# Optimization experiments

Measured on AMD Instinct MI355X. Metric: run time of the kernel, lower is better.

The kernel has to match this reference:

```python
import jax, jax.numpy as jnp
import numpy as np

B, A, F, D, C = 256, 128, 512, 6, 512  # batch, max_atoms, atom_features, max_degree, conv_width


def setup_inputs() -> dict:
    key = jax.random.key(0)
    k1, k2, k3, k4 = jax.random.split(key, 4)
    atoms = jax.random.normal(k1, (B, A, F), dtype=jnp.float32)
    # neighbour indices in [0, A); pad entries beyond each atom's degree with -1
    neigh = jax.random.randint(k2, (B, A, D), 0, A)
    deg = jax.random.randint(k3, (B, A, 1), 0, D)  # degrees in 0..D-1
    bonds = jnp.where(jnp.arange(D)[None, None, :] < deg, neigh, -1)
    # one Dense(conv_width) per degree: stacked kernels [D, F, C] and biases [D, C]
    W = jax.random.normal(k4, (D, F, C), dtype=jnp.float32) * 0.02
    b = jnp.zeros((D, C), dtype=jnp.float32)
    return {"atoms": atoms, "bonds": bonds, "W": W, "b": b}


def reference(atoms, bonds, W, b):
    d_max = bonds.shape[-1]
    # per-atom degree = count of non -1 neighbour slots  [B, A, 1]
    degrees = jnp.sum(bonds != -1, axis=-1, keepdims=True)
    # shift lookup by 1 so that padded (-1) neighbours index a zero row
    padded = jnp.pad(atoms, ((0, 0), (1, 1), (0, 0)))  # [B, A+2, F]
    idx = bonds + 1  # [B, A, D]
    # per-sample gather of neighbour features -> [B, A, D, F]
    neigh_feats = jax.vmap(lambda ref, i: ref[i])(padded, idx)
    summed = jnp.sum(neigh_feats, axis=2) + atoms  # [B, A, F]
    # apply all degree-specific dense layers, then mask-select by degree
    dense = jnp.einsum('baf,dfc->badc', summed, W) + b  # [B, A, D, C]
    masks = (degrees[..., None] == jnp.arange(d_max).reshape(1, 1, d_max, 1)).astype(dense.dtype)
    return jnp.sum(dense * masks, axis=2)  # [B, A, C]
```

## Files before the change

### kernel.cpp

```cpp
#include <hip/hip_runtime.h>
#include <hip/hip_bf16.h>


#define NB 256
#define NA 128
#define NF 512
#define ND 6
#define NC 512
#define NATOMS (NB * NA)

typedef __attribute__((ext_vector_type(8))) short frag8;
typedef __attribute__((ext_vector_type(4))) float f32x4;

static __device__ inline unsigned short f2bu(float f) {
    __hip_bfloat16 h = __float2bfloat16(f);
    return *reinterpret_cast<unsigned short*>(&h);
}
static __device__ inline unsigned int pack2(float a, float b) {
    return (unsigned int)f2bu(a) | ((unsigned int)f2bu(b) << 16);
}
static __device__ inline void async16(const void* g, void* l) {
    __builtin_amdgcn_global_load_lds(
        (const __attribute__((address_space(1))) void*)g,
        (__attribute__((address_space(3))) void*)l, 16, 0, 0);
}

#define PREP_T 1536
#define PREP_B (PREP_T + 32)
#define PREP_S (PREP_B + NATOMS / 4)

__global__ __launch_bounds__(256) void prep(
    const float* __restrict__ atoms, const int* __restrict__ bonds,
    const float* __restrict__ W, __hip_bfloat16* __restrict__ Wt,
    __hip_bfloat16* __restrict__ summed, int* __restrict__ counts,
    int* __restrict__ bucket) {
    const int blk = blockIdx.x;
    const int tid = threadIdx.x;

    if (blk < PREP_T) {
        __shared__ float t[32][33];
        const int tx = tid & 31, ty = tid >> 5;
        const int d   = blk >> 8;
        const int rem = blk & 255;
        const int c0  = (rem & 15) * 32;
        const int f0  = (rem >> 4) * 32;
        #pragma unroll
        for (int r = 0; r < 32; r += 8)
            t[ty + r][tx] = W[((size_t)(d * NF + f0 + ty + r)) * NC + c0 + tx];
        __syncthreads();
        #pragma unroll
        for (int r = 0; r < 32; r += 8)
            Wt[((size_t)(d * NC + c0 + ty + r)) * NF + f0 + tx] =
                __float2bfloat16(t[tx][ty + r]);
    } else if (blk < PREP_B) {
        __shared__ int lcnt[ND];
        __shared__ int lbase[ND];
        const int b = blk - PREP_T;
        if (tid < ND) lcnt[tid] = 0;
        __syncthreads();
        int deg[4], loc[4], gg[4];
        #pragma unroll
        for (int i = 0; i < 4; ++i) {
            int g = b * 1024 + i * 256 + tid;
            gg[i] = g;
            int dg = 0;
            #pragma unroll
            for (int j = 0; j < ND; ++j) dg += (bonds[g * ND + j] >= 0);
            deg[i] = dg;
            loc[i] = atomicAdd(&lcnt[dg], 1);
        }
        __syncthreads();
        if (tid < ND) lbase[tid] = atomicAdd(&counts[tid], lcnt[tid]);
        __syncthreads();
        #pragma unroll
        for (int i = 0; i < 4; ++i)
            bucket[deg[i] * NATOMS + lbase[deg[i]] + loc[i]] = gg[i];
    } else {
        const int wave = tid >> 6;
        const int lane = tid & 63;
        const int g    = (blk - PREP_B) * 4 + wave;
        const float4* a4 = (const float4*)atoms;

        int   nb[ND];
        float msk[ND];
        #pragma unroll
        for (int j = 0; j < ND; ++j) {
            int n = bonds[g * ND + j];
            msk[j] = (n >= 0) ? 1.0f : 0.0f;
            nb[j]  = (n >= 0) ? n : 0;
        }
        const int rowbase = g & ~(NA - 1);

        float4 s0 = a4[(size_t)g * 128 + 2 * lane];
        float4 s1 = a4[(size_t)g * 128 + 2 * lane + 1];
        float4 v0[ND], v1[ND];
        #pragma unroll
        for (int j = 0; j < ND; ++j) {
            const size_t base = (size_t)(rowbase + nb[j]) * 128 + 2 * lane;
            v0[j] = a4[base];
            v1[j] = a4[base + 1];
        }
        #pragma unroll
        for (int j = 0; j < ND; ++j) {
            s0.x = fmaf(v0[j].x, msk[j], s0.x); s0.y = fmaf(v0[j].y, msk[j], s0.y);
            s0.z = fmaf(v0[j].z, msk[j], s0.z); s0.w = fmaf(v0[j].w, msk[j], s0.w);
            s1.x = fmaf(v1[j].x, msk[j], s1.x); s1.y = fmaf(v1[j].y, msk[j], s1.y);
            s1.z = fmaf(v1[j].z, msk[j], s1.z); s1.w = fmaf(v1[j].w, msk[j], s1.w);
        }
        uint4 o;
        o.x = pack2(s0.x, s0.y); o.y = pack2(s0.z, s0.w);
        o.z = pack2(s1.x, s1.y); o.w = pack2(s1.z, s1.w);
        ((uint4*)summed)[(size_t)g * 64 + lane] = o;
    }
}

__global__ __launch_bounds__(256, 4) void gemm_deg(
    const __hip_bfloat16* __restrict__ summed, const __hip_bfloat16* __restrict__ Wt,
    const float* __restrict__ bias, const int* __restrict__ counts,
    const int* __restrict__ bucket, float* __restrict__ out) {
    const int bx = blockIdx.x;
    const int d  = bx % ND;
    const int n0 = (bx / ND) * 128;
    const int Md = counts[d];
    const int m0 = blockIdx.y * 128;
    if (m0 >= Md) return;

    __shared__ __align__(16) __hip_bfloat16 sA[2][128 * 32];
    __shared__ __align__(16) __hip_bfloat16 sB[2][128 * 32];
    __shared__ int sRows[128];

    const int tid = threadIdx.x;
    if (tid < 128) {
        int r = m0 + tid;
        sRows[tid] = (r < Md) ? bucket[d * NATOMS + r] : -1;
    }
    __syncthreads();

    const int lane = tid & 63;
    const int w    = tid >> 6;

    const int slot = lane & 3;
    int   rowc[2];
    size_t gA[2];
    int   segoff[2];
    #pragma unroll
    for (int c = 0; c < 2; ++c) {
        rowc[c] = c * 64 + w * 16 + (lane >> 2);
        int q = sRows[rowc[c]];
        gA[c] = (size_t)((q < 0) ? 0 : q) * (NF * 2);
        segoff[c] = (slot ^ ((rowc[c] >> 1) & 3)) * 16;
    }
    const char* smB = (const char*)summed;
    const char* wtB = (const char*)Wt + (size_t)(d * NC + n0) * (NF * 2);

    const int quad = lane >> 4, l16 = lane & 15;
    const int wy = w >> 1, wx = w & 1;

    f32x4 acc[4][4];
    #pragma unroll
    for (int i = 0; i < 4; ++i)
        #pragma unroll
        for (int j = 0; j < 4; ++j) acc[i][j] = (f32x4)0.0f;

    int offA[4], offB[4];
    #pragma unroll
    for (int i = 0; i < 4; ++i) {
        const int Ra = wy * 64 + i * 16 + l16;
        offA[i] = Ra * 32 + (quad ^ ((Ra >> 1) & 3)) * 8;
        const int Rb = wx * 64 + i * 16 + l16;
        offB[i] = Rb * 32 + (quad ^ ((Rb >> 1) & 3)) * 8;
    }

    #define STAGE(kt, p)                                                         \
        {                                                                        \
            const int kb = (kt) * 64;     \
            _Pragma("unroll")                                                    \
            for (int c = 0; c < 2; ++c) {                                        \
                async16(smB + gA[c] + kb + segoff[c],                            \
                        &sA[p][c * 2048 + w * 512]);                             \
                async16(wtB + (size_t)rowc[c] * (NF * 2) + kb + segoff[c],       \
                        &sB[p][c * 2048 + w * 512]);                             \
            }                                                                    \
        }

    STAGE(0, 0)
    #pragma unroll
    for (int kt = 0; kt < 16; ++kt) {
        const int p = kt & 1;
        __syncthreads();
        if (kt < 15) STAGE(kt + 1, 1 - p)
        frag8 aF[4], bF[4];
        #pragma unroll
        for (int i = 0; i < 4; ++i) aF[i] = *(const frag8*)&sA[p][offA[i]];
        #pragma unroll
        for (int j = 0; j < 4; ++j) bF[j] = *(const frag8*)&sB[p][offB[j]];
        #pragma unroll
        for (int i = 0; i < 4; ++i)
            #pragma unroll
            for (int j = 0; j < 4; ++j)
                acc[i][j] = __builtin_amdgcn_mfma_f32_16x16x32_bf16(
                    aF[i], bF[j], acc[i][j], 0, 0, 0);
    }
    #undef STAGE

    #pragma unroll
    for (int j = 0; j < 4; ++j) {
        const int n = n0 + wx * 64 + j * 16 + l16;
        const float bv = bias[d * NC + n];
        #pragma unroll
        for (int i = 0; i < 4; ++i) {
            #pragma unroll
            for (int r = 0; r < 4; ++r) {
                const int tr = wy * 64 + i * 16 + quad * 4 + r;
                const int g  = sRows[tr];
                if (g >= 0)
                    out[(size_t)g * NC + n] = acc[i][j][r] + bv;
            }
        }
    }
}

extern "C" void kernel_launch(void* const* d_in, const int* in_sizes, int n_in,
                              void* d_out, int out_size, void* d_ws, size_t ws_size,
                              hipStream_t stream) {
    const float* atoms = (const float*)d_in[0];
    const int*   bonds = (const int*)d_in[1];
    const float* W     = (const float*)d_in[2];
    const float* bias  = (const float*)d_in[3];
    float* out = (float*)d_out;

    char* ws = (char*)d_ws;
    int* counts = (int*)ws;
    int* bucket = (int*)(ws + 1024);
    __hip_bfloat16* Wt     = (__hip_bfloat16*)(ws + 1024 + 786432);
    __hip_bfloat16* summed = (__hip_bfloat16*)(ws + 1024 + 786432 + 3145728);

    hipMemsetAsync(counts, 0, 1024, stream);

    prep<<<PREP_S, 256, 0, stream>>>(atoms, bonds, W, Wt, summed, counts, bucket);

    gemm_deg<<<dim3(24, NATOMS / 128), 256, 0, stream>>>(
        summed, Wt, bias, counts, bucket, out);
}
```

Before: 184.4 us.

## Write summed features pre-permuted by degree bucket so GEMM reads contiguous rows

Bucketing moves into its own kernel, which also records each atom's degree and position within its bucket. The prep kernel uses these to write each summed row directly into a degree-sorted contiguous buffer, and it now handles two atoms per wave. The degree GEMM then loads A rows from consecutive addresses via a prefix offset instead of gathering rows scattered through the bucket indirection. This costs an extra kernel launch and serialises bucketing ahead of the gather/sum stage.

```diff
diff --git a/kernel.cpp b/kernel.cpp
--- a/kernel.cpp
+++ b/kernel.cpp
@@ -25,15 +25,45 @@
         (__attribute__((address_space(3))) void*)l, 16, 0, 0);
 }
 
+__global__ __launch_bounds__(256) void bucket_atoms(
+    const int* __restrict__ bonds, int* __restrict__ counts,
+    int* __restrict__ bucket, int* __restrict__ pdeg, int* __restrict__ ppos) {
+    __shared__ int lcnt[ND];
+    __shared__ int lbase[ND];
+    const int tid = threadIdx.x;
+    if (tid < ND) lcnt[tid] = 0;
+    __syncthreads();
+    int deg[4], loc[4], gg[4];
+    #pragma unroll
+    for (int i = 0; i < 4; ++i) {
+        int g = blockIdx.x * 1024 + i * 256 + tid;
+        gg[i] = g;
+        int dg = 0;
+        #pragma unroll
+        for (int j = 0; j < ND; ++j) dg += (bonds[g * ND + j] >= 0);
+        deg[i] = dg;
+        loc[i] = atomicAdd(&lcnt[dg], 1);
+    }
+    __syncthreads();
+    if (tid < ND) lbase[tid] = atomicAdd(&counts[tid], lcnt[tid]);
+    __syncthreads();
+    #pragma unroll
+    for (int i = 0; i < 4; ++i) {
+        int p = lbase[deg[i]] + loc[i];
+        bucket[deg[i] * NATOMS + p] = gg[i];
+        pdeg[gg[i]] = deg[i];
+        ppos[gg[i]] = p;
+    }
+}
+
 #define PREP_T 1536
-#define PREP_B (PREP_T + 32)
-#define PREP_S (PREP_B + NATOMS / 4)
+#define PREP_S (PREP_T + NATOMS / 8)
 
 __global__ __launch_bounds__(256) void prep(
     const float* __restrict__ atoms, const int* __restrict__ bonds,
     const float* __restrict__ W, __hip_bfloat16* __restrict__ Wt,
-    __hip_bfloat16* __restrict__ summed, int* __restrict__ counts,
-    int* __restrict__ bucket) {
+    __hip_bfloat16* __restrict__ summedP, const int* __restrict__ counts,
+    const int* __restrict__ pdeg, const int* __restrict__ ppos) {
     const int blk = blockIdx.x;
     const int tid = threadIdx.x;
 
@@ -52,70 +82,57 @@
         for (int r = 0; r < 32; r += 8)
             Wt[((size_t)(d * NC + c0 + ty + r)) * NF + f0 + tx] =
                 __float2bfloat16(t[tx][ty + r]);
-    } else if (blk < PREP_B) {
-        __shared__ int lcnt[ND];
-        __shared__ int lbase[ND];
-        const int b = blk - PREP_T;
-        if (tid < ND) lcnt[tid] = 0;
-        __syncthreads();
-        int deg[4], loc[4], gg[4];
-        #pragma unroll
-        for (int i = 0; i < 4; ++i) {
-            int g = b * 1024 + i * 256 + tid;
-            gg[i] = g;
-            int dg = 0;
-            #pragma unroll
-            for (int j = 0; j < ND; ++j) dg += (bonds[g * ND + j] >= 0);
-            deg[i] = dg;
-            loc[i] = atomicAdd(&lcnt[dg], 1);
-        }
-        __syncthreads();
-        if (tid < ND) lbase[tid] = atomicAdd(&counts[tid], lcnt[tid]);
-        __syncthreads();
-        #pragma unroll
-        for (int i = 0; i < 4; ++i)
-            bucket[deg[i] * NATOMS + lbase[deg[i]] + loc[i]] = gg[i];
     } else {
         const int wave = tid >> 6;
         const int lane = tid & 63;
-        const int g    = (blk - PREP_B) * 4 + wave;
+        const int g0   = (blk - PREP_T) * 8 + wave * 2;
         const float4* a4 = (const float4*)atoms;
 
-        int   nb[ND];
-        float msk[ND];
-        #pragma unroll
-        for (int j = 0; j < ND; ++j) {
-            int n = bonds[g * ND + j];
-            msk[j] = (n >= 0) ? 1.0f : 0.0f;
-            nb[j]  = (n >= 0) ? n : 0;
+        #pragma unroll
+        for (int a = 0; a < 2; ++a) {
+            const int g = g0 + a;
+            int   nb[ND];
+            float msk[ND];
+            #pragma unroll
+            for (int j = 0; j < ND; ++j) {
+                int n = bonds[g * ND + j];
+                msk[j] = (n >= 0) ? 1.0f : 0.0f;
+                nb[j]  = (n >= 0) ? n : 0;
+            }
+            const int rowbase = g & ~(NA - 1);
+
+            float4 s0 = a4[(size_t)g * 128 + 2 * lane];
+            float4 s1 = a4[(size_t)g * 128 + 2 * lane + 1];
+            float4 v0[ND], v1[ND];
+            #pragma unroll
+            for (int j = 0; j < ND; ++j) {
+                const size_t base = (size_t)(rowbase + nb[j]) * 128 + 2 * lane;
+                v0[j] = a4[base];
+                v1[j] = a4[base + 1];
+            }
+            #pragma unroll
+            for (int j = 0; j < ND; ++j) {
+                s0.x = fmaf(v0[j].x, msk[j], s0.x); s0.y = fmaf(v0[j].y, msk[j], s0.y);
+                s0.z = fmaf(v0[j].z, msk[j], s0.z); s0.w = fmaf(v0[j].w, msk[j], s0.w);
+                s1.x = fmaf(v1[j].x, msk[j], s1.x); s1.y = fmaf(v1[j].y, msk[j], s1.y);
+                s1.z = fmaf(v1[j].z, msk[j], s1.z); s1.w = fmaf(v1[j].w, msk[j], s1.w);
+            }
+
+            const int dg  = pdeg[g];
+            const int pos = ppos[g];
+            int pref = 0;
+            for (int i = 0; i < dg; ++i) pref += counts[i];
+
+            uint4 o;
+            o.x = pack2(s0.x, s0.y); o.y = pack2(s0.z, s0.w);
+            o.z = pack2(s1.x, s1.y); o.w = pack2(s1.z, s1.w);
+            ((uint4*)summedP)[(size_t)(pref + pos) * 64 + lane] = o;
         }
-        const int rowbase = g & ~(NA - 1);
-
-        float4 s0 = a4[(size_t)g * 128 + 2 * lane];
-        float4 s1 = a4[(size_t)g * 128 + 2 * lane + 1];
-        float4 v0[ND], v1[ND];
-        #pragma unroll
-        for (int j = 0; j < ND; ++j) {
-            const size_t base = (size_t)(rowbase + nb[j]) * 128 + 2 * lane;
-            v0[j] = a4[base];
-            v1[j] = a4[base + 1];
-        }
-        #pragma unroll
-        for (int j = 0; j < ND; ++j) {
-            s0.x = fmaf(v0[j].x, msk[j], s0.x); s0.y = fmaf(v0[j].y, msk[j], s0.y);
-            s0.z = fmaf(v0[j].z, msk[j], s0.z); s0.w = fmaf(v0[j].w, msk[j], s0.w);
-            s1.x = fmaf(v1[j].x, msk[j], s1.x); s1.y = fmaf(v1[j].y, msk[j], s1.y);
-            s1.z = fmaf(v1[j].z, msk[j], s1.z); s1.w = fmaf(v1[j].w, msk[j], s1.w);
-        }
-        uint4 o;
-        o.x = pack2(s0.x, s0.y); o.y = pack2(s0.z, s0.w);
-        o.z = pack2(s1.x, s1.y); o.w = pack2(s1.z, s1.w);
-        ((uint4*)summed)[(size_t)g * 64 + lane] = o;
     }
 }
 
 __global__ __launch_bounds__(256, 4) void gemm_deg(
-    const __hip_bfloat16* __restrict__ summed, const __hip_bfloat16* __restrict__ Wt,
+    const __hip_bfloat16* __restrict__ summedP, const __hip_bfloat16* __restrict__ Wt,
     const float* __restrict__ bias, const int* __restrict__ counts,
     const int* __restrict__ bucket, float* __restrict__ out) {
     const int bx = blockIdx.x;
@@ -124,6 +141,8 @@
     const int Md = counts[d];
     const int m0 = blockIdx.y * 128;
     if (m0 >= Md) return;
+    int pref = 0;
+    for (int i = 0; i < d; ++i) pref += counts[i];
 
     __shared__ __align__(16) __hip_bfloat16 sA[2][128 * 32];
     __shared__ __align__(16) __hip_bfloat16 sB[2][128 * 32];
@@ -140,17 +159,18 @@
     const int w    = tid >> 6;
 
     const int slot = lane & 3;
-    int   rowc[2];
+    int    rowc[2];
     size_t gA[2];
-    int   segoff[2];
+    int    segoff[2];
     #pragma unroll
     for (int c = 0; c < 2; ++c) {
         rowc[c] = c * 64 + w * 16 + (lane >> 2);
-        int q = sRows[rowc[c]];
-        gA[c] = (size_t)((q < 0) ? 0 : q) * (NF * 2);
+        int pr  = pref + m0 + rowc[c];
+        if (pr > NATOMS - 1) pr = NATOMS - 1;
+        gA[c] = (size_t)pr * (NF * 2);
         segoff[c] = (slot ^ ((rowc[c] >> 1) & 3)) * 16;
     }
-    const char* smB = (const char*)summed;
+    const char* smB = (const char*)summedP;
     const char* wtB = (const char*)Wt + (size_t)(d * NC + n0) * (NF * 2);
 
     const int quad = lane >> 4, l16 = lane & 15;
@@ -232,13 +252,17 @@
     char* ws = (char*)d_ws;
     int* counts = (int*)ws;
     int* bucket = (int*)(ws + 1024);
-    __hip_bfloat16* Wt     = (__hip_bfloat16*)(ws + 1024 + 786432);
-    __hip_bfloat16* summed = (__hip_bfloat16*)(ws + 1024 + 786432 + 3145728);
+    int* pdeg   = (int*)(ws + 1024 + 786432);
+    int* ppos   = (int*)(ws + 1024 + 786432 + 131072);
+    __hip_bfloat16* Wt      = (__hip_bfloat16*)(ws + 1049600);
+    __hip_bfloat16* summedP = (__hip_bfloat16*)(ws + 1049600 + 3145728);
 
     hipMemsetAsync(counts, 0, 1024, stream);
 
-    prep<<<PREP_S, 256, 0, stream>>>(atoms, bonds, W, Wt, summed, counts, bucket);
+    bucket_atoms<<<NATOMS / 1024, 256, 0, stream>>>(bonds, counts, bucket, pdeg, ppos);
+
+    prep<<<PREP_S, 256, 0, stream>>>(atoms, bonds, W, Wt, summedP, counts, pdeg, ppos);
 
     gemm_deg<<<dim3(24, NATOMS / 128), 256, 0, stream>>>(
-        summed, Wt, bias, counts, bucket, out);
-}
+        summedP, Wt, bias, counts, bucket, out);
+}
```

Result: slower. 188.7 us (+2.3%).
